# Performance work log

Measured on AMD Instinct MI355X. Metric: run time of the kernel, lower is better.

## Reference

```python
import jax, jax.numpy as jnp
import numpy as np
from jax import lax

V, B, C, H, W, D, G_DEF = 5, 2, 32, 128, 160, 32, 8


def _combine(proj):
    # proj: [B,2,4,4]; [:,0]=extrinsic, [:,1]=intrinsic; new[:, :3, :4] = K[:3,:3] @ E[:3,:4]
    ext, K = proj[:, 0], proj[:, 1]
    top = jnp.einsum('bij,bjk->bik', K[:, :3, :3], ext[:, :3, :4])
    return ext.at[:, :3, :4].set(top)


def _bilinear(img, x, y):
    # img [C,H,W]; x,y [N] pixel coords; zeros padding, align_corners=True (torch grid_sample)
    Ch, Hh, Wh = img.shape
    x0 = jnp.floor(x); y0 = jnp.floor(y)
    wx1 = x - x0; wy1 = y - y0
    def gather(xi, yi):
        valid = ((xi >= 0) & (xi <= Wh - 1) & (yi >= 0) & (yi <= Hh - 1)).astype(img.dtype)
        xc = jnp.clip(xi, 0, Wh - 1).astype(jnp.int32)
        yc = jnp.clip(yi, 0, Hh - 1).astype(jnp.int32)
        return img[:, yc, xc] * valid
    return (gather(x0, y0) * ((1 - wx1) * (1 - wy1)) + gather(x0 + 1, y0) * (wx1 * (1 - wy1))
            + gather(x0, y0 + 1) * ((1 - wx1) * wy1) + gather(x0 + 1, y0 + 1) * (wx1 * wy1))


def _conv3d(x, w, b, pad):
    y = lax.conv_general_dilated(x, w, (1, 1, 1), [(pad, pad)] * 3,
                                 dimension_numbers=('NCDHW', 'OIDHW', 'NCDHW'))
    return y + b[None, :, None, None, None]


def setup_inputs():
    key = jax.random.key(0)
    ks = jax.random.split(key, 8)
    features = jax.random.normal(ks[0], (V, B, C, H, W), jnp.float32)
    pm = np.zeros((B, V, 2, 4, 4), np.float32)
    for v in range(V):
        E = np.eye(4, dtype=np.float32); E[0, 3] = 0.05 * v  # small baseline along x
        K = np.eye(4, dtype=np.float32)
        K[0, 0] = K[1, 1] = float(W); K[0, 2] = W / 2.0; K[1, 2] = H / 2.0
        pm[:, v, 0] = E; pm[:, v, 1] = K
    proj_matrices = jnp.asarray(pm)
    d = jnp.linspace(1.0, 3.0, D, dtype=jnp.float32)
    depth_values = jnp.broadcast_to(d[None, :, None, None], (B, D, H, W))
    s = 0.1
    reg_w1 = jax.random.normal(ks[1], (8, G_DEF, 3, 3, 3), jnp.float32) * s
    reg_b1 = jnp.zeros((8,), jnp.float32)
    reg_w2 = jax.random.normal(ks[2], (1, 8, 3, 3, 3), jnp.float32) * s
    reg_b2 = jnp.zeros((1,), jnp.float32)
    pw_w1 = jax.random.normal(ks[3], (16, 1, 1, 1, 1), jnp.float32) * s
    pw_b1 = jnp.zeros((16,), jnp.float32)
    pw_w2 = jax.random.normal(ks[4], (8, 16, 1, 1, 1), jnp.float32) * s
    pw_b2 = jnp.zeros((8,), jnp.float32)
    pw_w3 = jax.random.normal(ks[5], (1, 8, 1, 1, 1), jnp.float32) * s
    pw_b3 = jnp.zeros((1,), jnp.float32)
    return dict(features=features, proj_matrices=proj_matrices, depth_values=depth_values,
                reg_w1=reg_w1, reg_b1=reg_b1, reg_w2=reg_w2, reg_b2=reg_b2,
                pw_w1=pw_w1, pw_b1=pw_b1, pw_w2=pw_w2, pw_b2=pw_b2,
                pw_w3=pw_w3, pw_b3=pw_b3, num_depth=D, G=G_DEF)


def reference(features, proj_matrices, depth_values, reg_w1, reg_b1, reg_w2, reg_b2,
              pw_w1, pw_b1, pw_w2, pw_b2, pw_w3, pw_b3, num_depth, G):
    Vn, Bn, Cn, Hn, Wn = features.shape
    Dn = num_depth
    ref_fea = features[0].reshape(Bn, G, Cn // G, Hn, Wn)
    ref_proj = _combine(proj_matrices[:, 0])
    ref_proj_inv = jnp.linalg.inv(ref_proj)
    ys, xs = jnp.meshgrid(jnp.arange(Hn, dtype=jnp.float32), jnp.arange(Wn, dtype=jnp.float32), indexing='ij')
    xyz = jnp.stack([xs.ravel(), ys.ravel(), jnp.ones(Hn * Wn, jnp.float32)], 0)  # [3, HW]
    sim_sum = 0.0; w_sum = 0.0; vws = []
    for v in range(1, Vn):  # fixed small view loop
        proj = jnp.einsum('bij,bjk->bik', _combine(proj_matrices[:, v]), ref_proj_inv)
        rot_xyz = jnp.einsum('bij,jn->bin', proj[:, :3, :3], xyz)  # [B,3,HW]
        pxyz = rot_xyz[:, :, None, :] * depth_values.reshape(Bn, 1, Dn, Hn * Wn) \
               + proj[:, :3, 3][:, :, None, None]  # [B,3,D,HW]
        # grid is computed under no_grad in torch -> stop_gradient
        x = lax.stop_gradient((pxyz[:, 0] / pxyz[:, 2]).reshape(Bn, -1))
        y = lax.stop_gradient((pxyz[:, 1] / pxyz[:, 2]).reshape(Bn, -1))
        warped = jax.vmap(_bilinear)(features[v], x, y).reshape(Bn, G, Cn // G, Dn, Hn, Wn)
        sim = (warped * ref_fea[:, :, :, None]).mean(2)  # [B,G,D,H,W] group correlation
        p = jax.nn.softmax(lax.stop_gradient(sim), axis=1)  # detached in torch
        ent = -(p * jnp.log(p + 1e-7)).sum(1, keepdims=True)  # [B,1,D,H,W]
        h = jax.nn.relu(_conv3d(ent, pw_w1, pw_b1, 0))
        h = jax.nn.relu(_conv3d(h, pw_w2, pw_b2, 0))
        vw = jax.nn.sigmoid(_conv3d(h, pw_w3, pw_b3, 0)).max(axis=2)  # [B,1,H,W]
        vws.append(vw)
        sim_sum = sim_sum + sim * vw[:, None]  # broadcast [B,1,1,H,W]
        w_sum = w_sum + vw[:, None]
    view_weights = jnp.concatenate(vws, axis=1)  # [B,V-1,H,W]
    similarity = sim_sum / (w_sum + 1e-6)
    h = jax.nn.relu(_conv3d(similarity, reg_w1, reg_b1, 1))
    prob_volume_pre = _conv3d(h, reg_w2, reg_b2, 1)[:, 0]  # [B,D,H,W]
    prob_volume = jax.nn.softmax(prob_volume_pre, axis=1)
    depth = (prob_volume * depth_values).sum(1)  # [B,H,W]
    pv = lax.stop_gradient(prob_volume)
    padded = jnp.pad(pv, ((0, 0), (1, 2), (0, 0), (0, 0)))
    # 4 * avg_pool3d(kernel=(4,1,1)) == sliding window sum over depth
    sum4 = lax.reduce_window(padded, 0.0, lax.add, (1, 4, 1, 1), (1, 1, 1, 1), 'VALID')
    didx = jnp.clip((pv * jnp.arange(Dn, dtype=pv.dtype)[None, :, None, None]).sum(1).astype(jnp.int32), 0, Dn - 1)
    photometric_confidence = jnp.take_along_axis(sum4, didx[:, None], axis=1)[:, 0]
    return depth, photometric_confidence, view_weights, prob_volume_pre, similarity
```

## Files before the change

kernel.cpp:

```cpp
#include <hip/hip_runtime.h>
#include <hip/hip_bf16.h>
#include <hip/hip_fp16.h>

#define V_  5
#define B_  2
#define C_  32
#define H_  128
#define W_  160
#define D_  32
#define G_  8
#define HW_  (H_*W_)
#define DHW_ (D_*HW_)

#define LOG2E_ 1.4426950408889634f
#define LN2_   0.6931471805599453f
#define LN8_   2.0794415416798357f

typedef _Float16 h8 __attribute__((ext_vector_type(8)));
typedef _Float16 h4 __attribute__((ext_vector_type(4)));
typedef _Float16 h2 __attribute__((ext_vector_type(2)));
typedef float    f4 __attribute__((ext_vector_type(4)));

__device__ inline float fdot2f(h2 a, h2 b, float c) {
#if __has_builtin(__builtin_amdgcn_fdot2)
    return __builtin_amdgcn_fdot2(a, b, c, false);
#else
    return fmaf((float)a[0], (float)b[0], fmaf((float)a[1], (float)b[1], c));
#endif
}


__device__ inline void combine_mat(const float* m, float out[4][4]) {
    const float* ext = m;
    const float* K   = m + 16;
    for (int r = 0; r < 4; ++r)
        for (int c = 0; c < 4; ++c)
            out[r][c] = ext[r*4 + c];
    for (int r = 0; r < 3; ++r)
        for (int c = 0; c < 4; ++c) {
            float s = 0.f;
            for (int k = 0; k < 3; ++k) s += K[r*4 + k] * ext[k*4 + c];
            out[r][c] = s;
        }
}

__device__ inline void invert4(const float Ain[4][4], float Inv[4][4]) {
    float A[4][4];
    for (int r = 0; r < 4; ++r)
        for (int c = 0; c < 4; ++c) {
            A[r][c]   = Ain[r][c];
            Inv[r][c] = (r == c) ? 1.f : 0.f;
        }
    for (int k = 0; k < 4; ++k) {
        int p = k; float best = fabsf(A[k][k]);
        for (int r = k + 1; r < 4; ++r) {
            float v = fabsf(A[r][k]);
            if (v > best) { best = v; p = r; }
        }
        if (p != k) {
            for (int j = 0; j < 4; ++j) {
                float t = A[k][j]; A[k][j] = A[p][j]; A[p][j] = t;
                t = Inv[k][j]; Inv[k][j] = Inv[p][j]; Inv[p][j] = t;
            }
        }
        float dinv = 1.f / A[k][k];
        for (int j = 0; j < 4; ++j) { A[k][j] *= dinv; Inv[k][j] *= dinv; }
        for (int r = 0; r < 4; ++r) {
            if (r == k) continue;
            float f = A[r][k];
            for (int j = 0; j < 4; ++j) {
                A[r][j]  -= f * A[k][j];
                Inv[r][j] -= f * Inv[k][j];
            }
        }
    }
}

__global__ __launch_bounds__(1024) void k_transpose(
    const float* __restrict__ in, _Float16* __restrict__ out,
    const float* __restrict__ pm,
    const float* __restrict__ pw_w1, const float* __restrict__ pw_b1,
    const float* __restrict__ pw_w2, const float* __restrict__ pw_b2,
    const float* __restrict__ pw_w3, const float* __restrict__ pw_b3,
    const float* __restrict__ reg_w1, const float* __restrict__ reg_w2,
    float* __restrict__ proj_ws, float* __restrict__ tabw,
    _Float16* __restrict__ wh1, _Float16* __restrict__ wh2)
{
    __shared__ float s[32][33];
    const int tx = threadIdx.x, ty = threadIdx.y;
    const int tid = ty * 32 + tx;
    const int hw0 = blockIdx.x * 32;
    const int vb  = blockIdx.y;
    s[ty][tx] = in[(vb * 32 + ty) * HW_ + hw0 + tx];
    __syncthreads();
    if (tid < 256) {
        int hw = tid >> 3, q = tid & 7;
        h4 hv;
        #pragma unroll
        for (int i = 0; i < 4; ++i) hv[i] = (_Float16)s[q*4 + i][hw];
        *(h4*)(out + ((size_t)vb * HW_ + hw0 + hw) * 32 + q*4) = hv;
    }

    if (blockIdx.x != 0 || blockIdx.y != 0) return;

    if (tid < B_) {
        int b = tid;
        float C0[4][4], C0inv[4][4];
        combine_mat(pm + (b * V_ + 0) * 32, C0);
        invert4(C0, C0inv);
        for (int v = 1; v < V_; ++v) {
            float Cv[4][4];
            combine_mat(pm + (b * V_ + v) * 32, Cv);
            float* o = proj_ws + (b * 4 + (v - 1)) * 12;
            for (int r = 0; r < 3; ++r)
                for (int c = 0; c < 4; ++c) {
                    float sacc = 0.f;
                    for (int k = 0; k < 4; ++k) sacc += Cv[r][k] * C0inv[k][c];
                    o[r*4 + c] = sacc;
                }
        }
    }
    for (int i = tid; i < 36*16*8; i += 1024) {
        int ic = i & 7; int m = (i >> 3) & 15; int slot = i >> 7;
        int wx = slot & 3; int grp = slot >> 2;
        wh1[i] = (_Float16)((wx < 3 && m < 8) ? reg_w1[(m*8 + ic)*27 + grp*3 + wx] : 0.f);
    }
    for (int i = tid; i < 36*8; i += 1024) {
        int ic = i & 7; int slot = i >> 3;
        int wx = slot & 3; int grp = slot >> 2;
        wh2[i] = (_Float16)((wx < 3) ? reg_w2[ic*27 + grp*3 + wx] : 0.f);
    }
    float ent = (float)tid * (LN8_ / 1023.0f);
    float h2v[8];
    #pragma unroll
    for (int jj = 0; jj < 8; ++jj) h2v[jj] = pw_b2[jj];
    for (int k = 0; k < 16; ++k) {
        float h1 = fmaxf(ent * pw_w1[k] + pw_b1[k], 0.f);
        #pragma unroll
        for (int jj = 0; jj < 8; ++jj) h2v[jj] += pw_w2[jj*16 + k] * h1;
    }
    float o3 = pw_b3[0];
    #pragma unroll
    for (int jj = 0; jj < 8; ++jj) o3 += pw_w3[jj] * fmaxf(h2v[jj], 0.f);
    tabw[tid] = 1.f / (1.f + expf(-o3));
}

__global__ __launch_bounds__(1024) void k_main(
    const _Float16* __restrict__ featT,
    const float* __restrict__ depthv,
    const float* __restrict__ proj_ws,
    const float* __restrict__ tabw,
    float* __restrict__ out_vw,
    float* __restrict__ out_sim,
    _Float16* __restrict__ simh)
{
    const int tid = threadIdx.x;
    const int wv   = tid >> 6;
    const int lane = tid & 63;
    const int j    = lane >> 5;
    const int d    = lane & 31;
    const int pxl  = wv * 2 + j;
    const int w0 = blockIdx.x * 32;
    const int h  = blockIdx.y;
    const int b  = blockIdx.z;
    const int w  = w0 + pxl;
    const int p  = h * W_ + w;

    __shared__ float tab_s[1024];
    __shared__ float proj_s[48];
    __shared__ float s_sim[G_][32][33];

    tab_s[tid] = tabw[tid];
    if (tid < 48) proj_s[tid] = proj_ws[b * 48 + tid];
    __syncthreads();

    const h8* rp = (const h8*)(featT + ((size_t)b * HW_ + p) * 32);
    h8 r8[4];
    #pragma unroll
    for (int cc = 0; cc < 4; ++cc) r8[cc] = rp[cc];

    const float depth = depthv[(b * D_ + d) * HW_ + p];
    const float xf = (float)w, yf = (float)h;

    float simsum[G_];
    #pragma unroll
    for (int g = 0; g < G_; ++g) simsum[g] = 0.f;
    float wsum = 0.f;

    for (int v = 1; v < V_; ++v) {
        const float* P = &proj_s[(v - 1) * 12];
        float px = (P[0]*xf + P[1]*yf + P[2])  * depth + P[3];
        float py = (P[4]*xf + P[5]*yf + P[6])  * depth + P[7];
        float pz = (P[8]*xf + P[9]*yf + P[10]) * depth + P[11];
        float rz = __builtin_amdgcn_rcpf(pz);
        float xs = px * rz;
        float ys = py * rz;

        float xr = rintf(xs);
        float yr = rintf(ys);
        xs = (fabsf(xs - xr) < 1e-4f) ? xr : xs;
        ys = (fabsf(ys - yr) < 1e-4f) ? yr : ys;

        float x0 = floorf(xs), y0 = floorf(ys);
        float wx1 = xs - x0,  wy1 = ys - y0;
        float wx0 = 1.f - wx1, wy0 = 1.f - wy1;

        bool vx0 = (x0 >= 0.f)     && (x0 <= (float)(W_-1));
        bool vx1 = (x0+1.f >= 0.f) && (x0+1.f <= (float)(W_-1));
        bool vy0 = (y0 >= 0.f)     && (y0 <= (float)(H_-1));
        bool vy1 = (y0+1.f >= 0.f) && (y0+1.f <= (float)(H_-1));

        int xc0 = (int)fminf(fmaxf(x0,     0.f), (float)(W_-1));
        int xc1 = (int)fminf(fmaxf(x0+1.f, 0.f), (float)(W_-1));
        int yc0 = (int)fminf(fmaxf(y0,     0.f), (float)(H_-1));
        int yc1 = (int)fminf(fmaxf(y0+1.f, 0.f), (float)(H_-1));

        float w00 = (vx0 && vy0) ? (wx0 * wy0) : 0.f;
        float w01 = (vx1 && vy0) ? (wx1 * wy0) : 0.f;
        float w10 = (vx0 && vy1) ? (wx0 * wy1) : 0.f;
        float w11 = (vx1 && vy1) ? (wx1 * wy1) : 0.f;

        const _Float16* vbp = featT + (size_t)(v * B_ + b) * HW_ * 32;

        float sim[G_];
        #pragma unroll
        for (int g = 0; g < G_; ++g) sim[g] = 0.f;

        bool top = __any(w00 > 0.f || w01 > 0.f);
        bool bot = __any(w10 > 0.f || w11 > 0.f);

        if (top) {
            h2 w00h = { (_Float16)w00, (_Float16)w00 };
            h2 w01h = { (_Float16)w01, (_Float16)w01 };
            const h8* t00 = (const h8*)(vbp + (size_t)(yc0 * W_ + xc0) * 32);
            const h8* t01 = (const h8*)(vbp + (size_t)(yc0 * W_ + xc1) * 32);
            #pragma unroll
            for (int cc = 0; cc < 4; ++cc) {
                h8 a = t00[cc], bb = t01[cc];
                const h2* ap = (const h2*)&a;
                const h2* bp = (const h2*)&bb;
                const h2* rv2 = (const h2*)&r8[cc];
                #pragma unroll
                for (int jp = 0; jp < 4; ++jp) {
                    h2 fv = ap[jp] * w00h + bp[jp] * w01h;
                    int g = cc*2 + (jp >> 1);
                    sim[g] = fdot2f(fv, rv2[jp], sim[g]);
                }
            }
        }
        if (bot) {
            h2 w10h = { (_Float16)w10, (_Float16)w10 };
            h2 w11h = { (_Float16)w11, (_Float16)w11 };
            const h8* t10 = (const h8*)(vbp + (size_t)(yc1 * W_ + xc0) * 32);
            const h8* t11 = (const h8*)(vbp + (size_t)(yc1 * W_ + xc1) * 32);
            #pragma unroll
            for (int cc = 0; cc < 4; ++cc) {
                h8 cq = t10[cc], dq = t11[cc];
                const h2* cp = (const h2*)&cq;
                const h2* dp = (const h2*)&dq;
                const h2* rv2 = (const h2*)&r8[cc];
                #pragma unroll
                for (int jp = 0; jp < 4; ++jp) {
                    h2 fv = cp[jp] * w10h + dp[jp] * w11h;
                    int g = cc*2 + (jp >> 1);
                    sim[g] = fdot2f(fv, rv2[jp], sim[g]);
                }
            }
        }

        #pragma unroll
        for (int g = 0; g < G_; ++g) sim[g] *= 0.25f;

        float m = sim[0];
        #pragma unroll
        for (int g = 1; g < G_; ++g) m = fmaxf(m, sim[g]);
        float es = 0.f, edot = 0.f;
        #pragma unroll
        for (int g = 0; g < G_; ++g) {
            float e = exp2f((sim[g] - m) * LOG2E_);
            es += e;
            edot = fmaf(e, sim[g], edot);
        }
        float inv_es = __builtin_amdgcn_rcpf(es);
        float ent = m + log2f(es) * LN2_ - edot * inv_es;

        float t = ent * (1023.0f / LN8_);
        t = fminf(fmaxf(t, 0.f), 1022.999f);
        int it = (int)t;
        float fr = t - (float)it;
        float lo = tab_s[it], hi = tab_s[it + 1];
        float sig = fmaf(hi - lo, fr, lo);

        float mv = sig;
        #pragma unroll
        for (int k = 16; k >= 1; k >>= 1)
            mv = fmaxf(mv, __shfl_xor(mv, k, 64));
        if (d == 0)
            out_vw[(b * 4 + (v - 1)) * HW_ + p] = mv;

        #pragma unroll
        for (int g = 0; g < G_; ++g) simsum[g] = fmaf(sim[g], mv, simsum[g]);
        wsum += mv;
    }

    float wn = __builtin_amdgcn_rcpf(wsum + 1e-6f);
    #pragma unroll
    for (int g = 0; g < G_; ++g) s_sim[g][d][pxl] = simsum[g] * wn;
    __syncthreads();

    const int tx = tid & 31;
    const int ty = tid >> 5;
    float* so = out_sim + (size_t)b * G_ * DHW_ + ty * HW_ + h * W_ + w0 + tx;
    h8 hv;
    #pragma unroll
    for (int g = 0; g < G_; ++g) {
        float val = s_sim[g][ty][tx];
        so[(size_t)g * DHW_] = val;
        hv[g] = (_Float16)val;
    }
    *(h8*)(simh + ((size_t)(b * D_ + ty) * HW_ + h * W_ + w0 + tx) * 8) = hv;
}


__global__ __launch_bounds__(256) void k_conv1m(
    const _Float16* __restrict__ in,
    const _Float16* __restrict__ wh,
    const float* __restrict__ bias,
    _Float16* __restrict__ outh)
{
    __shared__ _Float16 halo[6*10*34*8 + 8];
    const int tid = threadIdx.x;
    const int w0 = blockIdx.x * 32;
    const int h0 = blockIdx.y * 8;
    const int z  = blockIdx.z;
    const int b  = z >> 3;
    const int d0 = (z & 7) * 4;

    for (int pos = tid; pos < 2040; pos += 256) {
        int wx = pos % 34; int r = pos / 34; int hy = r % 10; int dz = r / 10;
        int gw = w0 + wx - 1, gh = h0 + hy - 1, gd = d0 + dz - 1;
        uint4 val = make_uint4(0u, 0u, 0u, 0u);
        if (gw >= 0 && gw < W_ && gh >= 0 && gh < H_ && gd >= 0 && gd < D_)
            val = *(const uint4*)(in + (((size_t)(b*D_ + gd)*H_ + gh)*W_ + gw)*8);
        *(uint4*)(halo + pos*8) = val;
    }
    if (tid == 0) *(uint4*)(halo + 6*10*34*8) = make_uint4(0u, 0u, 0u, 0u);

    const int wave = tid >> 6, lane = tid & 63;
    const int n = lane & 15, q = lane >> 4;

    h8 afrag[9];
    #pragma unroll
    for (int grp = 0; grp < 9; ++grp)
        afrag[grp] = *(const h8*)(wh + ((grp*4 + q)*16 + n)*8);

    f4 binit;
    #pragma unroll
    for (int reg = 0; reg < 4; ++reg)
        binit[reg] = (q < 2) ? bias[q*4 + reg] : 0.f;

    __syncthreads();

    const int lane_off = (n + q) * 16;

    #pragma unroll
    for (int it = 0; it < 4; ++it) {
        int t = wave*4 + it;
        int h_row = t >> 1, whalf = t & 1;
        const char* base = (const char*)halo + h_row*544 + whalf*256 + lane_off;
        #pragma unroll
        for (int dout = 0; dout < 4; ++dout) {
            f4 acc = binit;
            #pragma unroll
            for (int dz = 0; dz < 3; ++dz) {
                #pragma unroll
                for (int hy = 0; hy < 3; ++hy) {
                    h8 bfrag = *(const h8*)(base + (((dout + dz)*10 + hy)*544));
                    acc = __builtin_amdgcn_mfma_f32_16x16x32_f16(afrag[dz*3 + hy], bfrag, acc, 0, 0, 0);
                }
            }
            if (q < 2) {
                h4 hv;
                #pragma unroll
                for (int reg = 0; reg < 4; ++reg) hv[reg] = (_Float16)fmaxf(acc[reg], 0.f);
                *(h4*)(outh + (((size_t)(b*D_ + d0 + dout)*H_ + h0 + h_row)*W_ + w0 + whalf*16 + n)*8 + q*4) = hv;
            }
        }
    }
}

__global__ __launch_bounds__(256) void k_conv2m(
    const _Float16* __restrict__ in,
    const _Float16* __restrict__ wh,
    const float* __restrict__ bias,
    float* __restrict__ out)
{
    __shared__ _Float16 halo[6*10*34*8 + 8];
    const int tid = threadIdx.x;
    const int w0 = blockIdx.x * 32;
    const int h0 = blockIdx.y * 8;
    const int z  = blockIdx.z;
    const int b  = z >> 3;
    const int d0 = (z & 7) * 4;

    for (int pos = tid; pos < 2040; pos += 256) {
        int wx = pos % 34; int r = pos / 34; int hy = r % 10; int dz = r / 10;
        int gw = w0 + wx - 1, gh = h0 + hy - 1, gd = d0 + dz - 1;
        uint4 val = make_uint4(0u, 0u, 0u, 0u);
        if (gw >= 0 && gw < W_ && gh >= 0 && gh < H_ && gd >= 0 && gd < D_)
            val = *(const uint4*)(in + (((size_t)(b*D_ + gd)*H_ + gh)*W_ + gw)*8);
        *(uint4*)(halo + pos*8) = val;
    }
    if (tid == 0) *(uint4*)(halo + 6*10*34*8) = make_uint4(0u, 0u, 0u, 0u);

    const int wave = tid >> 6, lane = tid & 63;
    const int n = lane & 15, q = lane >> 4;

    h8 afrag[9];
    #pragma unroll
    for (int grp = 0; grp < 9; ++grp) {
        h8 a;
        #pragma unroll
        for (int e = 0; e < 8; ++e) a[e] = (_Float16)0.f;
        if (n == 0) a = *(const h8*)(wh + (grp*4 + q)*8);
        afrag[grp] = a;
    }
    const float b0 = bias[0];

    __syncthreads();

    const int lane_off = (n + q) * 16;

    #pragma unroll
    for (int it = 0; it < 4; ++it) {
        int t = wave*4 + it;
        int h_row = t >> 1, whalf = t & 1;
        const char* base = (const char*)halo + h_row*544 + whalf*256 + lane_off;
        #pragma unroll
        for (int dout = 0; dout < 4; ++dout) {
            f4 acc;
            acc[0] = (q == 0) ? b0 : 0.f;
            acc[1] = 0.f; acc[2] = 0.f; acc[3] = 0.f;
            #pragma unroll
            for (int dz = 0; dz < 3; ++dz) {
                #pragma unroll
                for (int hy = 0; hy < 3; ++hy) {
                    h8 bfrag = *(const h8*)(base + (((dout + dz)*10 + hy)*544));
                    acc = __builtin_amdgcn_mfma_f32_16x16x32_f16(afrag[dz*3 + hy], bfrag, acc, 0, 0, 0);
                }
            }
            if (q == 0)
                out[(((size_t)(b*D_ + d0 + dout)*H_ + h0 + h_row)*W_ + w0 + whalf*16 + n)] = acc[0];
        }
    }
}

__global__ __launch_bounds__(256) void k_final(
    const float* __restrict__ pvp,
    const float* __restrict__ depthv,
    float* __restrict__ out_depth,
    float* __restrict__ out_conf)
{
    int i = blockIdx.x * 256 + threadIdx.x;
    if (i >= B_ * HW_) return;
    int b = i / HW_;
    int p = i - b * HW_;

    const float* pp = pvp + b * DHW_ + p;
    const float* dv = depthv + b * DHW_ + p;

    float x[D_];
    float m = -3.4e38f;
    #pragma unroll
    for (int d = 0; d < D_; ++d) { x[d] = pp[d * HW_]; m = fmaxf(m, x[d]); }
    float s = 0.f;
    #pragma unroll
    for (int d = 0; d < D_; ++d) { x[d] = exp2f((x[d] - m) * LOG2E_); s += x[d]; }
    float inv = 1.f / s;

    float dep = 0.f, fd = 0.f;
    #pragma unroll
    for (int d = 0; d < D_; ++d) {
        float pv = x[d] * inv;
        x[d] = pv;
        dep = fmaf(pv, dv[d * HW_], dep);
        fd  = fmaf(pv, (float)d, fd);
    }
    int di = (int)fd;
    di = di < 0 ? 0 : (di > D_ - 1 ? D_ - 1 : di);
    float conf = 0.f;
    #pragma unroll
    for (int k = 0; k < 4; ++k) {
        int idx = di - 1 + k;
        if (idx >= 0 && idx < D_) conf += x[idx];
    }
    out_depth[i] = dep;
    out_conf[i]  = conf;
}

extern "C" void kernel_launch(void* const* d_in, const int* in_sizes, int n_in,
                              void* d_out, int out_size, void* d_ws, size_t ws_size,
                              hipStream_t stream) {
    const float* feat   = (const float*)d_in[0];
    const float* pm     = (const float*)d_in[1];
    const float* depthv = (const float*)d_in[2];
    const float* reg_w1 = (const float*)d_in[3];
    const float* reg_b1 = (const float*)d_in[4];
    const float* reg_w2 = (const float*)d_in[5];
    const float* reg_b2 = (const float*)d_in[6];
    const float* pw_w1  = (const float*)d_in[7];
    const float* pw_b1  = (const float*)d_in[8];
    const float* pw_w2  = (const float*)d_in[9];
    const float* pw_b2  = (const float*)d_in[10];
    const float* pw_w3  = (const float*)d_in[11];
    const float* pw_b3  = (const float*)d_in[12];

    float* out = (float*)d_out;
    float* out_depth = out;
    float* out_conf  = out + B_*HW_;
    float* out_vw    = out + 2*B_*HW_;
    float* out_pvp   = out_vw + B_*4*HW_;
    float* out_sim   = out_pvp + B_*DHW_;

    float* ws      = (float*)d_ws;
    float* proj_ws = ws;
    float* tabw    = ws + 128;
    _Float16* wh1  = (_Float16*)(ws + 1152);
    _Float16* wh2  = (_Float16*)(ws + 3456);
    _Float16* featT = (_Float16*)(ws + 4736);
    _Float16* hidh  = (_Float16*)(ws + 4736);
    _Float16* simh  = (_Float16*)(ws + 4736 + 5242880);

    hipLaunchKernelGGL(k_transpose, dim3(HW_/32, V_*B_), dim3(32, 32), 0, stream,
                       feat, featT,
                       pm, pw_w1, pw_b1, pw_w2, pw_b2, pw_w3, pw_b3,
                       reg_w1, reg_w2, proj_ws, tabw, wh1, wh2);

    hipLaunchKernelGGL(k_main, dim3(W_/32, H_, B_), dim3(1024), 0, stream,
                       featT, depthv, proj_ws, tabw, out_vw, out_sim, simh);

    hipLaunchKernelGGL(k_conv1m, dim3(W_/32, H_/8, B_*D_/4), dim3(256), 0, stream,
                       simh, wh1, reg_b1, hidh);

    hipLaunchKernelGGL(k_conv2m, dim3(W_/32, H_/8, B_*D_/4), dim3(256), 0, stream,
                       hidh, wh2, reg_b2, out_pvp);

    hipLaunchKernelGGL(k_final, dim3((B_*HW_ + 255)/256), dim3(256), 0, stream,
                       out_pvp, depthv, out_depth, out_conf);
}
```

Measured before the change: 211.4 us.

## Stage reprojected feature row segment in LDS for single-row warps in k_main

k_main now precomputes the projected sample coordinates for all views and stores packed indices and fp16 weights in shared memory. Per-view min/max bounds are gathered with atomics to decide whether the whole block samples a single source row within a 64-pixel span with no bottom-row weight. When that holds, that row segment is cooperatively loaded into LDS and the bilinear taps read from LDS instead of scattered global loads. Depth values are also staged through shared memory. The change adds extra barriers, atomics and LDS use (about 16KB more), which may reduce occupancy, and the fast path only applies for near-rectified geometry like the test cameras.

```diff
diff --git a/kernel.cpp b/kernel.cpp
--- a/kernel.cpp
+++ b/kernel.cpp
@@ -1,6 +1,7 @@
 #include <hip/hip_runtime.h>
 #include <hip/hip_bf16.h>
 #include <hip/hip_fp16.h>
+#include <stdint.h>
 
 #define V_  5
 #define B_  2
@@ -145,7 +146,39 @@
     tabw[tid] = 1.f / (1.f + expf(-o3));
 }
 
-__global__ __launch_bounds__(1024) void k_main(
+
+struct C5 { float w00, w01, w10, w11; int xc0, xc1, yc0, yc1; };
+
+__device__ inline C5 proj_coords(const float* __restrict__ P, float xf, float yf, float depth) {
+    C5 c;
+    float px = (P[0]*xf + P[1]*yf + P[2])  * depth + P[3];
+    float py = (P[4]*xf + P[5]*yf + P[6])  * depth + P[7];
+    float pz = (P[8]*xf + P[9]*yf + P[10]) * depth + P[11];
+    float rz = __builtin_amdgcn_rcpf(pz);
+    float xs = px * rz;
+    float ys = py * rz;
+    float xr = rintf(xs), yr = rintf(ys);
+    xs = (fabsf(xs - xr) < 1e-4f) ? xr : xs;
+    ys = (fabsf(ys - yr) < 1e-4f) ? yr : ys;
+    float x0 = floorf(xs), y0 = floorf(ys);
+    float wx1 = xs - x0,  wy1 = ys - y0;
+    float wx0 = 1.f - wx1, wy0 = 1.f - wy1;
+    bool vx0 = (x0 >= 0.f)     && (x0 <= (float)(W_-1));
+    bool vx1 = (x0+1.f >= 0.f) && (x0+1.f <= (float)(W_-1));
+    bool vy0 = (y0 >= 0.f)     && (y0 <= (float)(H_-1));
+    bool vy1 = (y0+1.f >= 0.f) && (y0+1.f <= (float)(H_-1));
+    c.xc0 = (int)fminf(fmaxf(x0,     0.f), (float)(W_-1));
+    c.xc1 = (int)fminf(fmaxf(x0+1.f, 0.f), (float)(W_-1));
+    c.yc0 = (int)fminf(fmaxf(y0,     0.f), (float)(H_-1));
+    c.yc1 = (int)fminf(fmaxf(y0+1.f, 0.f), (float)(H_-1));
+    c.w00 = (vx0 && vy0) ? (wx0 * wy0) : 0.f;
+    c.w01 = (vx1 && vy0) ? (wx1 * wy0) : 0.f;
+    c.w10 = (vx0 && vy1) ? (wx0 * wy1) : 0.f;
+    c.w11 = (vx1 && vy1) ? (wx1 * wy1) : 0.f;
+    return c;
+}
+
+__global__ __launch_bounds__(1024, 8) void k_main(
     const _Float16* __restrict__ featT,
     const float* __restrict__ depthv,
     const float* __restrict__ proj_ws,
@@ -168,10 +201,75 @@
 
     __shared__ float tab_s[1024];
     __shared__ float proj_s[48];
-    __shared__ float s_sim[G_][32][33];
+    __shared__ __align__(16) float s_sim[G_][32][33];
+    __shared__ __align__(16) uint32_t stageu[4][1024];
+    __shared__ float s_dep[32][33];
+    __shared__ int fin[4][6];
 
     tab_s[tid] = tabw[tid];
     if (tid < 48) proj_s[tid] = proj_ws[b * 48 + tid];
+    { int dd = tid >> 5, pp = tid & 31;
+      s_dep[dd][pp] = depthv[(b * D_ + dd) * HW_ + h * W_ + w0 + pp]; }
+    if (tid < 24) {
+        int vv = tid / 6, f = tid % 6;
+        int val;
+        if (f == 0 || f == 2) val = 0x7fffffff;
+        else if (f == 1 || f == 3) val = (int)0x80000000;
+        else if (f == 4) val = 1;
+        else val = 0;
+        fin[vv][f] = val;
+    }
+    __syncthreads();
+
+    const float depth = s_dep[d][pxl];
+    const float xf = (float)w, yf = (float)h;
+
+    #pragma unroll
+    for (int v = 1; v < V_; ++v) {
+        C5 c = proj_coords(&proj_s[(v - 1) * 12], xf, yf, depth);
+        uint32_t pk = (uint32_t)c.xc0 | ((uint32_t)c.xc1 << 16);
+        h2 wp = { (_Float16)c.w00, (_Float16)c.w01 };
+        uint32_t wpu = __builtin_bit_cast(uint32_t, wp);
+        ((uint2*)s_sim)[(v - 1) * 1024 + tid] = make_uint2(pk, wpu);
+
+        int xmn = c.xc0, xmx = c.xc1;
+        #pragma unroll
+        for (int k = 32; k >= 1; k >>= 1) {
+            int a = __shfl_xor(xmn, k, 64); xmn = a < xmn ? a : xmn;
+            int bmx = __shfl_xor(xmx, k, 64); xmx = bmx > xmx ? bmx : xmx;
+        }
+        int y0f = __shfl(c.yc0, 0, 64);
+        bool rowu = __all(c.yc0 == y0f);
+        bool bnw  = __any(c.w10 > 0.f || c.w11 > 0.f);
+        if (lane == 0) {
+            atomicMin(&fin[v-1][0], xmn);
+            atomicMax(&fin[v-1][1], xmx);
+            atomicMin(&fin[v-1][2], y0f);
+            atomicMax(&fin[v-1][3], y0f);
+            if (!rowu) fin[v-1][4] = 0;
+            if (bnw)   fin[v-1][5] = 1;
+        }
+    }
+    __syncthreads();
+
+    #pragma unroll
+    for (int v = 1; v < V_; ++v) {
+        int fxmin = fin[v-1][0];
+        int yrow  = fin[v-1][2];
+        bool fast = fin[v-1][4] && !fin[v-1][5] &&
+                    (fin[v-1][2] == fin[v-1][3]) && (fin[v-1][1] - fxmin < 64);
+        if (fast) {
+            int rec0 = yrow * W_ + fxmin;
+            int rec  = rec0 + (tid >> 4);
+            uint32_t val = 0u;
+            if (rec < HW_) {
+                const uint32_t* src = (const uint32_t*)featT +
+                    ((size_t)(v * B_ + b) * HW_ + (size_t)rec0) * 16;
+                val = src[tid];
+            }
+            stageu[v-1][((((tid >> 2) & 3) << 6) | (tid >> 4)) * 4 + (tid & 3)] = val;
+        }
+    }
     __syncthreads();
 
     const h8* rp = (const h8*)(featT + ((size_t)b * HW_ + p) * 32);
@@ -179,91 +277,86 @@
     #pragma unroll
     for (int cc = 0; cc < 4; ++cc) r8[cc] = rp[cc];
 
-    const float depth = depthv[(b * D_ + d) * HW_ + p];
-    const float xf = (float)w, yf = (float)h;
-
     float simsum[G_];
     #pragma unroll
     for (int g = 0; g < G_; ++g) simsum[g] = 0.f;
     float wsum = 0.f;
 
+    #pragma unroll
     for (int v = 1; v < V_; ++v) {
-        const float* P = &proj_s[(v - 1) * 12];
-        float px = (P[0]*xf + P[1]*yf + P[2])  * depth + P[3];
-        float py = (P[4]*xf + P[5]*yf + P[6])  * depth + P[7];
-        float pz = (P[8]*xf + P[9]*yf + P[10]) * depth + P[11];
-        float rz = __builtin_amdgcn_rcpf(pz);
-        float xs = px * rz;
-        float ys = py * rz;
-
-        float xr = rintf(xs);
-        float yr = rintf(ys);
-        xs = (fabsf(xs - xr) < 1e-4f) ? xr : xs;
-        ys = (fabsf(ys - yr) < 1e-4f) ? yr : ys;
-
-        float x0 = floorf(xs), y0 = floorf(ys);
-        float wx1 = xs - x0,  wy1 = ys - y0;
-        float wx0 = 1.f - wx1, wy0 = 1.f - wy1;
-
-        bool vx0 = (x0 >= 0.f)     && (x0 <= (float)(W_-1));
-        bool vx1 = (x0+1.f >= 0.f) && (x0+1.f <= (float)(W_-1));
-        bool vy0 = (y0 >= 0.f)     && (y0 <= (float)(H_-1));
-        bool vy1 = (y0+1.f >= 0.f) && (y0+1.f <= (float)(H_-1));
-
-        int xc0 = (int)fminf(fmaxf(x0,     0.f), (float)(W_-1));
-        int xc1 = (int)fminf(fmaxf(x0+1.f, 0.f), (float)(W_-1));
-        int yc0 = (int)fminf(fmaxf(y0,     0.f), (float)(H_-1));
-        int yc1 = (int)fminf(fmaxf(y0+1.f, 0.f), (float)(H_-1));
-
-        float w00 = (vx0 && vy0) ? (wx0 * wy0) : 0.f;
-        float w01 = (vx1 && vy0) ? (wx1 * wy0) : 0.f;
-        float w10 = (vx0 && vy1) ? (wx0 * wy1) : 0.f;
-        float w11 = (vx1 && vy1) ? (wx1 * wy1) : 0.f;
-
-        const _Float16* vbp = featT + (size_t)(v * B_ + b) * HW_ * 32;
-
         float sim[G_];
         #pragma unroll
         for (int g = 0; g < G_; ++g) sim[g] = 0.f;
 
-        bool top = __any(w00 > 0.f || w01 > 0.f);
-        bool bot = __any(w10 > 0.f || w11 > 0.f);
-
-        if (top) {
-            h2 w00h = { (_Float16)w00, (_Float16)w00 };
-            h2 w01h = { (_Float16)w01, (_Float16)w01 };
-            const h8* t00 = (const h8*)(vbp + (size_t)(yc0 * W_ + xc0) * 32);
-            const h8* t01 = (const h8*)(vbp + (size_t)(yc0 * W_ + xc1) * 32);
-            #pragma unroll
-            for (int cc = 0; cc < 4; ++cc) {
-                h8 a = t00[cc], bb = t01[cc];
-                const h2* ap = (const h2*)&a;
-                const h2* bp = (const h2*)&bb;
-                const h2* rv2 = (const h2*)&r8[cc];
+        int fxmin = fin[v-1][0];
+        bool fast = fin[v-1][4] && !fin[v-1][5] &&
+                    (fin[v-1][2] == fin[v-1][3]) && (fin[v-1][1] - fxmin < 64);
+
+        if (fast) {
+            uint2 sv = ((const uint2*)s_sim)[(v - 1) * 1024 + tid];
+            int xc0 = (int)(sv.x & 0xffffu), xc1 = (int)(sv.x >> 16);
+            h2 wp = __builtin_bit_cast(h2, sv.y);
+            bool top = __any(wp[0] > (_Float16)0.f || wp[1] > (_Float16)0.f);
+            if (top) {
+                h2 w00h = { wp[0], wp[0] };
+                h2 w01h = { wp[1], wp[1] };
+                const h8* sp = (const h8*)&stageu[v-1][0];
+                int xr0 = xc0 - fxmin, xr1 = xc1 - fxmin;
                 #pragma unroll
-                for (int jp = 0; jp < 4; ++jp) {
-                    h2 fv = ap[jp] * w00h + bp[jp] * w01h;
-                    int g = cc*2 + (jp >> 1);
-                    sim[g] = fdot2f(fv, rv2[jp], sim[g]);
+                for (int cc = 0; cc < 4; ++cc) {
+                    h8 a = sp[cc*64 + xr0], bb = sp[cc*64 + xr1];
+                    const h2* ap = (const h2*)&a;
+                    const h2* bp = (const h2*)&bb;
+                    const h2* rv2 = (const h2*)&r8[cc];
+                    #pragma unroll
+                    for (int jp = 0; jp < 4; ++jp) {
+                        h2 fv = ap[jp] * w00h + bp[jp] * w01h;
+                        int g = cc*2 + (jp >> 1);
+                        sim[g] = fdot2f(fv, rv2[jp], sim[g]);
+                    }
                 }
             }
-        }
-        if (bot) {
-            h2 w10h = { (_Float16)w10, (_Float16)w10 };
-            h2 w11h = { (_Float16)w11, (_Float16)w11 };
-            const h8* t10 = (const h8*)(vbp + (size_t)(yc1 * W_ + xc0) * 32);
-            const h8* t11 = (const h8*)(vbp + (size_t)(yc1 * W_ + xc1) * 32);
-            #pragma unroll
-            for (int cc = 0; cc < 4; ++cc) {
-                h8 cq = t10[cc], dq = t11[cc];
-                const h2* cp = (const h2*)&cq;
-                const h2* dp = (const h2*)&dq;
-                const h2* rv2 = (const h2*)&r8[cc];
+        } else {
+            C5 c = proj_coords(&proj_s[(v - 1) * 12], xf, yf, depth);
+            const _Float16* vbp = featT + (size_t)(v * B_ + b) * HW_ * 32;
+            bool top = __any(c.w00 > 0.f || c.w01 > 0.f);
+            bool bot = __any(c.w10 > 0.f || c.w11 > 0.f);
+            if (top) {
+                h2 w00h = { (_Float16)c.w00, (_Float16)c.w00 };
+                h2 w01h = { (_Float16)c.w01, (_Float16)c.w01 };
+                const h8* t00 = (const h8*)(vbp + (size_t)(c.yc0 * W_ + c.xc0) * 32);
+                const h8* t01 = (const h8*)(vbp + (size_t)(c.yc0 * W_ + c.xc1) * 32);
                 #pragma unroll
-                for (int jp = 0; jp < 4; ++jp) {
-                    h2 fv = cp[jp] * w10h + dp[jp] * w11h;
-                    int g = cc*2 + (jp >> 1);
-                    sim[g] = fdot2f(fv, rv2[jp], sim[g]);
+                for (int cc = 0; cc < 4; ++cc) {
+                    h8 a = t00[cc], bb = t01[cc];
+                    const h2* ap = (const h2*)&a;
+                    const h2* bp = (const h2*)&bb;
+                    const h2* rv2 = (const h2*)&r8[cc];
+                    #pragma unroll
+                    for (int jp = 0; jp < 4; ++jp) {
+                        h2 fv = ap[jp] * w00h + bp[jp] * w01h;
+                        int g = cc*2 + (jp >> 1);
+                        sim[g] = fdot2f(fv, rv2[jp], sim[g]);
+                    }
+                }
+            }
+            if (bot) {
+                h2 w10h = { (_Float16)c.w10, (_Float16)c.w10 };
+                h2 w11h = { (_Float16)c.w11, (_Float16)c.w11 };
+                const h8* t10 = (const h8*)(vbp + (size_t)(c.yc1 * W_ + c.xc0) * 32);
+                const h8* t11 = (const h8*)(vbp + (size_t)(c.yc1 * W_ + c.xc1) * 32);
+                #pragma unroll
+                for (int cc = 0; cc < 4; ++cc) {
+                    h8 cq = t10[cc], dq = t11[cc];
+                    const h2* cp = (const h2*)&cq;
+                    const h2* dp = (const h2*)&dq;
+                    const h2* rv2 = (const h2*)&r8[cc];
+                    #pragma unroll
+                    for (int jp = 0; jp < 4; ++jp) {
+                        h2 fv = cp[jp] * w10h + dp[jp] * w11h;
+                        int g = cc*2 + (jp >> 1);
+                        sim[g] = fdot2f(fv, rv2[jp], sim[g]);
+                    }
                 }
             }
         }
@@ -303,6 +396,8 @@
         wsum += mv;
     }
 
+    __syncthreads();
+
     float wn = __builtin_amdgcn_rcpf(wsum + 1e-6f);
     #pragma unroll
     for (int g = 0; g < G_; ++g) s_sim[g][d][pxl] = simsum[g] * wn;
@@ -320,7 +415,6 @@
     }
     *(h8*)(simh + ((size_t)(b * D_ + ty) * HW_ + h * W_ + w0 + tx) * 8) = hv;
 }
-
 
 __global__ __launch_bounds__(256) void k_conv1m(
     const _Float16* __restrict__ in,
```

Result: slower. 229.5 us (+8.5%).
